# Kernel tuning notes

Measured on AMD Instinct MI355X. Metric: run time of the kernel, lower is better.

The kernel has to match this reference:

```python
import jax, jax.numpy as jnp
import numpy as np

GRID = 14    # grid_size[0]
PATCH = 16   # patch_size[0]

def setup_inputs() -> dict:
    key = jax.random.key(0)
    x = jax.random.normal(key, (32, 96, 224, 224), dtype=jnp.float32)
    return {"x": x}

def reference(x):
    # x: [B, C, H, W] with H = W = GRID*PATCH
    B, C, H, W = x.shape
    g, p = GRID, PATCH
    # [B, C, gi, pi, gj, pj]
    t = x.reshape(B, C, g, p, g, p)
    # L2 norm over (C, gi, gj) for each intra-patch offset (pi, pj) -> [B, p, p]
    sq = jnp.sum(t * t, axis=(1, 2, 4))
    norms = jnp.sqrt(sq)
    # argmax over flattened (pi, pj), pj fastest -> matches torch reshape order
    idx = jnp.argmax(norms.reshape(B, p * p), axis=1)
    si = idx // p  # row shift
    sj = idx % p   # col shift
    # circular pad + translate-by-(si,sj) + crop == circular roll by (-si, -sj)
    out = jax.vmap(lambda xi, a, b: jnp.roll(xi, (-a, -b), axis=(1, 2)))(x, si, sj)
    return out
```

## Files before the change

kernel.cpp:

```cpp
#include <hip/hip_runtime.h>

#define H 224
#define W 224
#define B 32
#define C 96

typedef float nfloat4 __attribute__((ext_vector_type(4)));



template<int R>
__device__ __forceinline__ void roll_body(const float* __restrict__ xb,
                                          float* __restrict__ ob,
                                          int c0, int h0, int sh0,
                                          int q, int lane) {
    int v = lane + q;  if (v >= 56) v -= 56;
    int nl = lane + 1; if (nl >= 56) nl = 0;
    int sh = sh0;
    #pragma unroll
    for (int it = 0; it < 8; ++it) {
        int h = h0 + it * 4;
        const nfloat4* srow = (const nfloat4*)(xb + ((size_t)c0 * H + sh) * W);
        nfloat4*       drow = (nfloat4*)      (ob + ((size_t)c0 * H + h)  * W);
        nfloat4 a = __builtin_nontemporal_load(srow + v);
        nfloat4 o;
        if (R == 0) {
            o = a;
        } else {
            float nx = __shfl(a.x, nl);
            float ny = (R >= 2) ? __shfl(a.y, nl) : 0.0f;
            float nz = (R == 3) ? __shfl(a.z, nl) : 0.0f;
            if (R == 1) { o.x = a.y; o.y = a.z; o.z = a.w; o.w = nx; }
            if (R == 2) { o.x = a.z; o.y = a.w; o.z = nx;  o.w = ny; }
            if (R == 3) { o.x = a.w; o.y = nx;  o.z = ny;  o.w = nz; }
        }
        __builtin_nontemporal_store(o, drow + lane);
        sh += 4; if (sh >= H) sh -= H;
    }
}

__global__ void fused_kernel(const float* __restrict__ x, float* __restrict__ out,
                             float* __restrict__ nbuf,
                             int nStart, int nCount, int rStart, int rCount) {
    int wave = threadIdx.x >> 6;
    int lane = threadIdx.x & 63;

    if ((int)blockIdx.x < nCount * 128) {
        int b     = nStart + ((int)blockIdx.x >> 7);
        int sub   = blockIdx.x & 127;
        int pi    = sub >> 3;
        int slice = sub & 7;

        __shared__ float bins[16];
        if (threadIdx.x < 16) bins[threadIdx.x] = 0.0f;
        __syncthreads();

        if (lane < 56) {
            const float* base = x + (size_t)b * C * H * W;
            int c = slice * 12 + wave * 3;
            const size_t HW4 = (size_t)H * W / 4;
            const float4* p = (const float4*)(base + ((size_t)c * H + pi) * W);
            float a0=0.f,a1=0.f,a2=0.f,a3=0.f;
            float b0=0.f,b1=0.f,b2=0.f,b3=0.f;
            float c0_=0.f,c1=0.f,c2=0.f,c3=0.f;
            const size_t giStep = (size_t)16 * W / 4;
            for (int gi = 0; gi < 14; ++gi) {
                float4 va = p[lane];
                float4 vb = (p + HW4)[lane];
                float4 vc = (p + 2 * HW4)[lane];
                a0 += va.x * va.x; a1 += va.y * va.y; a2 += va.z * va.z; a3 += va.w * va.w;
                b0 += vb.x * vb.x; b1 += vb.y * vb.y; b2 += vb.z * vb.z; b3 += vb.w * vb.w;
                c0_ += vc.x * vc.x; c1 += vc.y * vc.y; c2 += vc.z * vc.z; c3 += vc.w * vc.w;
                p += giStep;
            }
            a0 += b0 + c0_;
            a1 += b1 + c1;
            a2 += b2 + c2;
            a3 += b3 + c3;
            int bse = (lane & 3) << 2;
            atomicAdd(&bins[bse + 0], a0);
            atomicAdd(&bins[bse + 1], a1);
            atomicAdd(&bins[bse + 2], a2);
            atomicAdd(&bins[bse + 3], a3);
        }
        __syncthreads();
        if (threadIdx.x < 16)
            nbuf[((b * 8 + slice) * 16 + pi) * 16 + threadIdx.x] = bins[threadIdx.x];
    } else {
        int rIdx  = blockIdx.x - nCount * 128;
        int b     = rStart + rIdx / 672;
        int local = rIdx % 672;

        const float* nb = nbuf + (size_t)b * 2048;
        int t = threadIdx.x;
        float v = 0.0f;
        #pragma unroll
        for (int s = 0; s < 8; ++s) v += nb[s * 256 + t];
        int idx = t;
        for (int off = 32; off > 0; off >>= 1) {
            float ov = __shfl_down(v, off);
            int   oi = __shfl_down(idx, off);
            if (ov > v || (ov == v && oi < idx)) { v = ov; idx = oi; }
        }
        __shared__ float wv[4];
        __shared__ int   wi[4];
        __shared__ int   ssi, ssj;
        if (lane == 0) { wv[wave] = v; wi[wave] = idx; }
        __syncthreads();
        if (threadIdx.x == 0) {
            float bv = wv[0]; int bi = wi[0];
            #pragma unroll
            for (int w = 1; w < 4; ++w)
                if (wv[w] > bv) { bv = wv[w]; bi = wi[w]; }
            ssi = bi >> 4; ssj = bi & 15;
        }
        __syncthreads();
        int si = ssi, sj = ssj;

        if (lane < 56) {
            int q = sj >> 2, r = sj & 3;
            int c0 = local / 7;
            int h0 = (local % 7) * 32 + wave;
            int sh0 = h0 + si; if (sh0 >= H) sh0 -= H;
            const float* xb = x   + (size_t)b * C * H * W;
            float*       ob = out + (size_t)b * C * H * W;
            switch (r) {
                case 0: roll_body<0>(xb, ob, c0, h0, sh0, q, lane); break;
                case 1: roll_body<1>(xb, ob, c0, h0, sh0, q, lane); break;
                case 2: roll_body<2>(xb, ob, c0, h0, sh0, q, lane); break;
                default: roll_body<3>(xb, ob, c0, h0, sh0, q, lane); break;
            }
        }
    }
}

extern "C" void kernel_launch(void* const* d_in, const int* in_sizes, int n_in,
                              void* d_out, int out_size, void* d_ws, size_t ws_size,
                              hipStream_t stream) {
    const float* x = (const float*)d_in[0];
    float* outp = (float*)d_out;
    float* nbuf = (float*)d_ws;

    const int GROUP = 4;
    const int NSTAGE = B / GROUP;
    for (int i = 0; i <= NSTAGE; ++i) {
        int nStart = GROUP * i;
        int nCount = (i < NSTAGE) ? GROUP : 0;
        int rStart = GROUP * (i - 1);
        int rCount = (i > 0) ? GROUP : 0;
        int blocks = nCount * 128 + rCount * 672;
        fused_kernel<<<blocks, 256, 0, stream>>>(x, outp, nbuf,
                                                 nStart, nCount, rStart, rCount);
    }
}
```

Measured before the change: 294.8 us.

## Split fused pipelined launches into separate norms and roll kernels

```diff
diff --git a/kernel.cpp b/kernel.cpp
--- a/kernel.cpp
+++ b/kernel.cpp
@@ -8,6 +8,51 @@
 typedef float nfloat4 __attribute__((ext_vector_type(4)));
 
 
+__global__ __launch_bounds__(256) void norms_kernel(const float* __restrict__ x,
+                                                    float* __restrict__ nbuf) {
+    int sub   = blockIdx.x;
+    int b     = blockIdx.y;
+    int pi    = sub >> 3;
+    int slice = sub & 7;
+    int wave  = threadIdx.x >> 6;
+    int lane  = threadIdx.x & 63;
+
+    __shared__ float bins[16];
+    if (threadIdx.x < 16) bins[threadIdx.x] = 0.0f;
+    __syncthreads();
+
+    if (lane < 56) {
+        const float* base = x + (size_t)b * C * H * W;
+        int c = slice * 12 + wave * 3;
+        const size_t HW4 = (size_t)H * W / 4;
+        const nfloat4* p = (const nfloat4*)(base + ((size_t)c * H + pi) * W);
+        float a0=0.f,a1=0.f,a2=0.f,a3=0.f;
+        float b0=0.f,b1=0.f,b2=0.f,b3=0.f;
+        float c0_=0.f,c1=0.f,c2=0.f,c3=0.f;
+        const size_t giStep = (size_t)16 * W / 4;
+        for (int gi = 0; gi < 14; ++gi) {
+            nfloat4 va = __builtin_nontemporal_load(p + lane);
+            nfloat4 vb = __builtin_nontemporal_load(p + HW4 + lane);
+            nfloat4 vc = __builtin_nontemporal_load(p + 2 * HW4 + lane);
+            a0 += va.x * va.x; a1 += va.y * va.y; a2 += va.z * va.z; a3 += va.w * va.w;
+            b0 += vb.x * vb.x; b1 += vb.y * vb.y; b2 += vb.z * vb.z; b3 += vb.w * vb.w;
+            c0_ += vc.x * vc.x; c1 += vc.y * vc.y; c2 += vc.z * vc.z; c3 += vc.w * vc.w;
+            p += giStep;
+        }
+        a0 += b0 + c0_;
+        a1 += b1 + c1;
+        a2 += b2 + c2;
+        a3 += b3 + c3;
+        int bse = (lane & 3) << 2;
+        atomicAdd(&bins[bse + 0], a0);
+        atomicAdd(&bins[bse + 1], a1);
+        atomicAdd(&bins[bse + 2], a2);
+        atomicAdd(&bins[bse + 3], a3);
+    }
+    __syncthreads();
+    if (threadIdx.x < 16)
+        nbuf[((b * 8 + slice) * 16 + pi) * 16 + threadIdx.x] = bins[threadIdx.x];
+}
 
 template<int R>
 __device__ __forceinline__ void roll_body(const float* __restrict__ xb,
@@ -39,97 +84,52 @@
     }
 }
 
-__global__ void fused_kernel(const float* __restrict__ x, float* __restrict__ out,
-                             float* __restrict__ nbuf,
-                             int nStart, int nCount, int rStart, int rCount) {
-    int wave = threadIdx.x >> 6;
-    int lane = threadIdx.x & 63;
+__global__ __launch_bounds__(256) void roll_kernel(const float* __restrict__ x,
+                                                   float* __restrict__ out,
+                                                   const float* __restrict__ nbuf) {
+    int local = blockIdx.x;
+    int b     = blockIdx.y;
+    int wave  = threadIdx.x >> 6;
+    int lane  = threadIdx.x & 63;
 
-    if ((int)blockIdx.x < nCount * 128) {
-        int b     = nStart + ((int)blockIdx.x >> 7);
-        int sub   = blockIdx.x & 127;
-        int pi    = sub >> 3;
-        int slice = sub & 7;
+    const float* nb = nbuf + (size_t)b * 2048;
+    int t = threadIdx.x;
+    float v = 0.0f;
+    #pragma unroll
+    for (int s = 0; s < 8; ++s) v += nb[s * 256 + t];
+    int idx = t;
+    for (int off = 32; off > 0; off >>= 1) {
+        float ov = __shfl_down(v, off);
+        int   oi = __shfl_down(idx, off);
+        if (ov > v || (ov == v && oi < idx)) { v = ov; idx = oi; }
+    }
+    __shared__ float wv[4];
+    __shared__ int   wi[4];
+    __shared__ int   ssi, ssj;
+    if (lane == 0) { wv[wave] = v; wi[wave] = idx; }
+    __syncthreads();
+    if (threadIdx.x == 0) {
+        float bv = wv[0]; int bi = wi[0];
+        #pragma unroll
+        for (int w = 1; w < 4; ++w)
+            if (wv[w] > bv) { bv = wv[w]; bi = wi[w]; }
+        ssi = bi >> 4; ssj = bi & 15;
+    }
+    __syncthreads();
+    int si = ssi, sj = ssj;
 
-        __shared__ float bins[16];
-        if (threadIdx.x < 16) bins[threadIdx.x] = 0.0f;
-        __syncthreads();
-
-        if (lane < 56) {
-            const float* base = x + (size_t)b * C * H * W;
-            int c = slice * 12 + wave * 3;
-            const size_t HW4 = (size_t)H * W / 4;
-            const float4* p = (const float4*)(base + ((size_t)c * H + pi) * W);
-            float a0=0.f,a1=0.f,a2=0.f,a3=0.f;
-            float b0=0.f,b1=0.f,b2=0.f,b3=0.f;
-            float c0_=0.f,c1=0.f,c2=0.f,c3=0.f;
-            const size_t giStep = (size_t)16 * W / 4;
-            for (int gi = 0; gi < 14; ++gi) {
-                float4 va = p[lane];
-                float4 vb = (p + HW4)[lane];
-                float4 vc = (p + 2 * HW4)[lane];
-                a0 += va.x * va.x; a1 += va.y * va.y; a2 += va.z * va.z; a3 += va.w * va.w;
-                b0 += vb.x * vb.x; b1 += vb.y * vb.y; b2 += vb.z * vb.z; b3 += vb.w * vb.w;
-                c0_ += vc.x * vc.x; c1 += vc.y * vc.y; c2 += vc.z * vc.z; c3 += vc.w * vc.w;
-                p += giStep;
-            }
-            a0 += b0 + c0_;
-            a1 += b1 + c1;
-            a2 += b2 + c2;
-            a3 += b3 + c3;
-            int bse = (lane & 3) << 2;
-            atomicAdd(&bins[bse + 0], a0);
-            atomicAdd(&bins[bse + 1], a1);
-            atomicAdd(&bins[bse + 2], a2);
-            atomicAdd(&bins[bse + 3], a3);
-        }
-        __syncthreads();
-        if (threadIdx.x < 16)
-            nbuf[((b * 8 + slice) * 16 + pi) * 16 + threadIdx.x] = bins[threadIdx.x];
-    } else {
-        int rIdx  = blockIdx.x - nCount * 128;
-        int b     = rStart + rIdx / 672;
-        int local = rIdx % 672;
-
-        const float* nb = nbuf + (size_t)b * 2048;
-        int t = threadIdx.x;
-        float v = 0.0f;
-        #pragma unroll
-        for (int s = 0; s < 8; ++s) v += nb[s * 256 + t];
-        int idx = t;
-        for (int off = 32; off > 0; off >>= 1) {
-            float ov = __shfl_down(v, off);
-            int   oi = __shfl_down(idx, off);
-            if (ov > v || (ov == v && oi < idx)) { v = ov; idx = oi; }
-        }
-        __shared__ float wv[4];
-        __shared__ int   wi[4];
-        __shared__ int   ssi, ssj;
-        if (lane == 0) { wv[wave] = v; wi[wave] = idx; }
-        __syncthreads();
-        if (threadIdx.x == 0) {
-            float bv = wv[0]; int bi = wi[0];
-            #pragma unroll
-            for (int w = 1; w < 4; ++w)
-                if (wv[w] > bv) { bv = wv[w]; bi = wi[w]; }
-            ssi = bi >> 4; ssj = bi & 15;
-        }
-        __syncthreads();
-        int si = ssi, sj = ssj;
-
-        if (lane < 56) {
-            int q = sj >> 2, r = sj & 3;
-            int c0 = local / 7;
-            int h0 = (local % 7) * 32 + wave;
-            int sh0 = h0 + si; if (sh0 >= H) sh0 -= H;
-            const float* xb = x   + (size_t)b * C * H * W;
-            float*       ob = out + (size_t)b * C * H * W;
-            switch (r) {
-                case 0: roll_body<0>(xb, ob, c0, h0, sh0, q, lane); break;
-                case 1: roll_body<1>(xb, ob, c0, h0, sh0, q, lane); break;
-                case 2: roll_body<2>(xb, ob, c0, h0, sh0, q, lane); break;
-                default: roll_body<3>(xb, ob, c0, h0, sh0, q, lane); break;
-            }
+    if (lane < 56) {
+        int q = sj >> 2, r = sj & 3;
+        int c0 = local / 7;
+        int h0 = (local % 7) * 32 + wave;
+        int sh0 = h0 + si; if (sh0 >= H) sh0 -= H;
+        const float* xb = x   + (size_t)b * C * H * W;
+        float*       ob = out + (size_t)b * C * H * W;
+        switch (r) {
+            case 0: roll_body<0>(xb, ob, c0, h0, sh0, q, lane); break;
+            case 1: roll_body<1>(xb, ob, c0, h0, sh0, q, lane); break;
+            case 2: roll_body<2>(xb, ob, c0, h0, sh0, q, lane); break;
+            default: roll_body<3>(xb, ob, c0, h0, sh0, q, lane); break;
         }
     }
 }
@@ -141,15 +141,6 @@
     float* outp = (float*)d_out;
     float* nbuf = (float*)d_ws;
 
-    const int GROUP = 4;
-    const int NSTAGE = B / GROUP;
-    for (int i = 0; i <= NSTAGE; ++i) {
-        int nStart = GROUP * i;
-        int nCount = (i < NSTAGE) ? GROUP : 0;
-        int rStart = GROUP * (i - 1);
-        int rCount = (i > 0) ? GROUP : 0;
-        int blocks = nCount * 128 + rCount * 672;
-        fused_kernel<<<blocks, 256, 0, stream>>>(x, outp, nbuf,
-                                                 nStart, nCount, rStart, rCount);
-    }
+    norms_kernel<<<dim3(128, 32), 256, 0, stream>>>(x, nbuf);
+    roll_kernel<<<dim3(672, 32), 256, 0, stream>>>(x, outp, nbuf);
 }
```

Result: no change. 293.4 us (-0.5%).
